# Optimization experiments

Measured on AMD Instinct MI355X. Metric: run time of the kernel, lower is better.

The kernel has to match this reference:

```python
import jax, jax.numpy as jnp
import numpy as np

B, C, H, W = 4, 256, 64, 64
INTER = max(1, C // 8)  # 32


def setup_inputs() -> dict:
    key = jax.random.key(0)
    ks = jax.random.split(key, 8)
    s = 0.02  # conv weight init scale
    return {
        "feat": jax.random.normal(ks[0], (B, C, H, W), jnp.float32),
        "edge": jax.random.normal(ks[1], (B, C, H, W), jnp.float32),
        "wq": jax.random.normal(ks[2], (INTER, C), jnp.float32) * s,
        "bq": jnp.zeros((INTER,), jnp.float32),
        "wk": jax.random.normal(ks[3], (INTER, C), jnp.float32) * s,
        "bk": jnp.zeros((INTER,), jnp.float32),
        "wv": jax.random.normal(ks[4], (C, C), jnp.float32) * s,
        "bv": jnp.zeros((C,), jnp.float32),
    }


def reference(feat, edge, wq, bq, wk, bk, wv, bv):
    b, c, h, w = feat.shape
    n = h * w
    # 1x1 convs as channel matmuls; flatten spatial dims to n = H*W tokens
    q = (jnp.einsum('ic,bchw->bihw', wq, feat) + bq[None, :, None, None]).reshape(b, -1, n)  # [B, inter, N]
    k = (jnp.einsum('ic,bchw->bihw', wk, edge) + bk[None, :, None, None]).reshape(b, -1, n)  # [B, inter, N]
    v = (jnp.einsum('oc,bchw->bohw', wv, edge) + bv[None, :, None, None]).reshape(b, c, n)   # [B, C, N]
    # scores[b, nq, nk] = sum_i q[b,i,nq] * k[b,i,nk]; softmax over nk
    attn = jax.nn.softmax(jnp.einsum('bin,bim->bnm', q, k), axis=-1)  # [B, N, N]
    # out[b,c,nq] = sum_m v[b,c,m] * attn[b,nq,m]
    out = jnp.einsum('bcm,bnm->bcn', v, attn).reshape(b, c, h, w)
    return out + feat
```

## Files before the change

### kernel.cpp

```cpp
#include <hip/hip_runtime.h>
#include <cstddef>

#define BB 4
#define CC 256
#define NN 4096
#define NI 32

typedef __attribute__((ext_vector_type(8))) short bf16x8;
typedef __attribute__((ext_vector_type(16))) float f32x16;
typedef __attribute__((ext_vector_type(4))) float f32x4;
typedef unsigned short ushort_t;
typedef unsigned int uint32;

typedef union { uint32 u[4]; bf16x8 v; } fragU;

__device__ __forceinline__ uint32 f2bf_bits(float f) {
    union { float f; uint32 u; } v; v.f = f;
    return (v.u + 0x7fffu + ((v.u >> 16) & 1u)) >> 16;
}
__device__ __forceinline__ uint32 pack2bf(float a, float b) {
    return f2bf_bits(a) | (f2bf_bits(b) << 16);
}
__device__ __forceinline__ uint32 pack2bf_t(float a, float b) {
    union { float f; uint32 u; } A, B; A.f = a; B.f = b;
    return (B.u & 0xFFFF0000u) | (A.u >> 16);
}

__device__ __forceinline__ size_t vfidx(int b, int n, int c) {
    return ((((size_t)b * (NN / 16) + (n >> 4)) * 2 + ((n >> 3) & 1)) * (CC * 8))
           + (size_t)c * 8 + (n & 7);
}

__global__ __launch_bounds__(256) void wconv_kernel(
    const float* __restrict__ wq, const float* __restrict__ wk,
    const float* __restrict__ wv,
    ushort_t* __restrict__ wqF, ushort_t* __restrict__ wkF,
    ushort_t* __restrict__ wvF)
{
    const int bid = blockIdx.x;
    const int t = threadIdx.x;
    if (bid < 64) {
        const int fi = bid * 256 + t;
        const int o  = fi >> 6;
        const int k4 = (fi & 63) * 4;
        const f32x4 x = *(const f32x4*)&wv[(size_t)o * CC + k4];
        const int kkg = k4 >> 4, hh = (k4 >> 3) & 1, j0 = k4 & 7;
        const int ot = o >> 5, lane = hh * 32 + (o & 31);
        uint2 p; p.x = pack2bf(x[0], x[1]); p.y = pack2bf(x[2], x[3]);
        *(uint2*)&wvF[((size_t)(ot * 16 + kkg) * 64 + lane) * 8 + j0] = p;
    } else {
        const int which = (bid - 64) >> 1;
        const int part  = (bid - 64) & 1;
        const float* src = which ? wk : wq;
        ushort_t* dst = which ? wkF : wqF;
#pragma unroll
        for (int p = 0; p < 4; ++p) {
            const int fi = part * 1024 + p * 256 + t;
            const int o  = fi >> 6;
            const int k4 = (fi & 63) * 4;
            const f32x4 x = *(const f32x4*)&src[(size_t)o * CC + k4];
            const int kkg = k4 >> 4, hh = (k4 >> 3) & 1, j0 = k4 & 7;
            const int lane = hh * 32 + (o & 31);
            uint2 pr; pr.x = pack2bf(x[0], x[1]); pr.y = pack2bf(x[2], x[3]);
            *(uint2*)&dst[((size_t)kkg * 64 + lane) * 8 + j0] = pr;
        }
    }
}

__global__ __launch_bounds__(256, 1) void proj_kernel(
    const float* __restrict__ feat, const float* __restrict__ edge,
    const ushort_t* __restrict__ wqF, const ushort_t* __restrict__ wkF,
    const ushort_t* __restrict__ wvF,
    const float* __restrict__ bq, const float* __restrict__ bk,
    const float* __restrict__ bv,
    ushort_t* __restrict__ qT, ushort_t* __restrict__ kT,
    ushort_t* __restrict__ vF)
{
    __shared__ __attribute__((aligned(16))) uint32 sF[4][2][64][4];
    __shared__ __attribute__((aligned(16))) uint32 sE[4][2][64][4];

    const int tid = threadIdx.x;
    const int b = blockIdx.y;
    const int n0 = blockIdx.x * 64;
    const int w = tid >> 6, lane = tid & 63;
    const int col = lane & 31, h = lane >> 5;

    const ushort_t* __restrict__ aQK = ((w < 2) ? wqF : wkF) + (size_t)lane * 8;
    const ushort_t* __restrict__ wvB0 = wvF + ((size_t)((2 * w + 0) * 16) * 64 + lane) * 8;
    const ushort_t* __restrict__ wvB1 = wvF + ((size_t)((2 * w + 1) * 16) * 64 + lane) * 8;
    const uint32* __restrict__ bSrc =
        (w == 0) ? &sF[0][0][lane][0] :
        (w == 1) ? &sF[0][1][lane][0] :
        (w == 2) ? &sE[0][0][lane][0] : &sE[0][1][lane][0];

    f32x16 accV[2][2];
    f32x16 accS;
#pragma unroll
    for (int r = 0; r < 16; ++r) {
        accS[r] = 0.f;
        accV[0][0][r] = 0.f; accV[0][1][r] = 0.f;
        accV[1][0][r] = 0.f; accV[1][1][r] = 0.f;
    }

    f32x4 rF[2][2], rE[2][2];

#pragma unroll
    for (int p = 0; p < 2; ++p) {
        const int pi = p * 256 + tid;
        const int m = pi >> 4, cidx = pi & 15;
        const size_t ga = ((size_t)(b * CC + 2 * m)) * NN + n0 + cidx * 4;
        rF[p][0] = *(const f32x4*)&feat[ga];
        rF[p][1] = *(const f32x4*)&feat[ga + NN];
        rE[p][0] = *(const f32x4*)&edge[ga];
        rE[p][1] = *(const f32x4*)&edge[ga + NN];
    }

    for (int ch = 0; ch < 4; ++ch) {
#pragma unroll
        for (int p = 0; p < 2; ++p) {
            const int pi = p * 256 + tid;
            const int m = pi >> 4, cidx = pi & 15;
            const int kk = m >> 3, hh = (m >> 2) & 1, ju = m & 3;
#pragma unroll
            for (int c = 0; c < 4; ++c) {
                const int cn = cidx * 4 + c;
                const int nt = cn >> 5, cl = cn & 31;
                sF[kk][nt][hh * 32 + cl][ju] = pack2bf(rF[p][0][c], rF[p][1][c]);
                sE[kk][nt][hh * 32 + cl][ju] = pack2bf(rE[p][0][c], rE[p][1][c]);
            }
        }
        __syncthreads();

        if (ch < 3) {
            const int c0 = (ch + 1) * 64;
#pragma unroll
            for (int p = 0; p < 2; ++p) {
                const int pi = p * 256 + tid;
                const int m = pi >> 4, cidx = pi & 15;
                const size_t ga = ((size_t)(b * CC + c0 + 2 * m)) * NN + n0 + cidx * 4;
                rF[p][0] = *(const f32x4*)&feat[ga];
                rF[p][1] = *(const f32x4*)&feat[ga + NN];
                rE[p][0] = *(const f32x4*)&edge[ga];
                rE[p][1] = *(const f32x4*)&edge[ga + NN];
            }
        }

#pragma unroll
        for (int kk = 0; kk < 4; ++kk) {
            const int kkg = ch * 4 + kk;
            const bf16x8 eA0 = *(const bf16x8*)&sE[kk][0][lane][0];
            const bf16x8 eA1 = *(const bf16x8*)&sE[kk][1][lane][0];
            const bf16x8 vB0 = *(const bf16x8*)&wvB0[(size_t)kkg * 512];
            const bf16x8 vB1 = *(const bf16x8*)&wvB1[(size_t)kkg * 512];
            const bf16x8 aS  = *(const bf16x8*)&aQK[(size_t)kkg * 512];
            const bf16x8 bS  = *(const bf16x8*)&bSrc[(size_t)kk * 512];
            accS = __builtin_amdgcn_mfma_f32_32x32x16_bf16(aS, bS, accS, 0, 0, 0);
            accV[0][0] = __builtin_amdgcn_mfma_f32_32x32x16_bf16(eA0, vB0, accV[0][0], 0, 0, 0);
            accV[0][1] = __builtin_amdgcn_mfma_f32_32x32x16_bf16(eA0, vB1, accV[0][1], 0, 0, 0);
            accV[1][0] = __builtin_amdgcn_mfma_f32_32x32x16_bf16(eA1, vB0, accV[1][0], 0, 0, 0);
            accV[1][1] = __builtin_amdgcn_mfma_f32_32x32x16_bf16(eA1, vB1, accV[1][1], 0, 0, 0);
        }
        __syncthreads();
    }

    {
        const float* bias = (w < 2) ? bq : bk;
        ushort_t* dst = (w < 2) ? qT : kT;
        const int nt = w & 1;
        const size_t base = ((size_t)b * NN + n0 + nt * 32 + col) * NI;
#pragma unroll
        for (int q = 0; q < 4; ++q) {
            const int i0 = 8 * q + 4 * h;
            const float x0 = accS[4 * q + 0] + bias[i0 + 0];
            const float x1 = accS[4 * q + 1] + bias[i0 + 1];
            const float x2 = accS[4 * q + 2] + bias[i0 + 2];
            const float x3 = accS[4 * q + 3] + bias[i0 + 3];
            uint2 pr; pr.x = pack2bf(x0, x1); pr.y = pack2bf(x2, x3);
            *(uint2*)&dst[base + i0] = pr;
        }
    }

#pragma unroll
    for (int cti = 0; cti < 2; ++cti) {
        const int o = (2 * w + cti) * 32 + col;
        const float vb = bv[o];
#pragma unroll
        for (int mt = 0; mt < 2; ++mt) {
#pragma unroll
            for (int q = 0; q < 4; ++q) {
                const int nst = n0 + mt * 32 + 8 * q + 4 * h;
                uint2 pr;
                pr.x = pack2bf(accV[mt][cti][4 * q + 0] + vb,
                               accV[mt][cti][4 * q + 1] + vb);
                pr.y = pack2bf(accV[mt][cti][4 * q + 2] + vb,
                               accV[mt][cti][4 * q + 3] + vb);
                *(uint2*)&vF[vfidx(b, nst, o)] = pr;
            }
        }
    }
}

__global__ __launch_bounds__(512, 2) void attn_kernel(
    const ushort_t* __restrict__ qT, const ushort_t* __restrict__ kT,
    const ushort_t* __restrict__ vF, const float* __restrict__ feat,
    float* __restrict__ out)
{
    __shared__ float red[4][64][33];
    __shared__ float lpart[4][2][32];
    __shared__ float linvS[64];

    const int tid  = threadIdx.x;
    const int b    = blockIdx.y;
    const int nq0  = blockIdx.x * 64;
    const int w    = tid >> 6;
    const int lane = tid & 63;
    const int col  = lane & 31;
    const int h    = lane >> 5;
    const int qs   = w & 1;
    const int kg   = w >> 1;

    bf16x8 bQ0, bQ1;
    {
        const size_t qb = ((size_t)b * NN + nq0 + qs * 32 + col) * NI + h * 8;
        bQ0 = *(const bf16x8*)&qT[qb];
        bQ1 = *(const bf16x8*)&qT[qb + 16];
    }

    f32x16 acc[8];
#pragma unroll
    for (int cs = 0; cs < 8; ++cs)
#pragma unroll
        for (int r = 0; r < 16; ++r) acc[cs][r] = 0.f;

    float lp = 0.f;

    const size_t kTb = (size_t)b * NN * NI;
    const int keybase = kg * 1024;

    for (int strip = 0; strip < 32; ++strip) {
        const int key0 = keybase + strip * 32;

        const size_t kb = kTb + (size_t)(key0 + col) * NI + h * 8;
        const bf16x8 aK0 = *(const bf16x8*)&kT[kb];
        const bf16x8 aK1 = *(const bf16x8*)&kT[kb + 16];

        f32x16 st;
#pragma unroll
        for (int r = 0; r < 16; ++r) st[r] = 0.f;
        st = __builtin_amdgcn_mfma_f32_32x32x16_bf16(aK0, bQ0, st, 0, 0, 0);
        st = __builtin_amdgcn_mfma_f32_32x32x16_bf16(aK1, bQ1, st, 0, 0, 0);

        float p[16]; float sum = 0.f;
#pragma unroll
        for (int r = 0; r < 16; ++r) { p[r] = __expf(st[r]); sum += p[r]; }
        lp += sum;

        uint32 pk[8];
#pragma unroll
        for (int j = 0; j < 8; ++j) pk[j] = pack2bf_t(p[2 * j], p[2 * j + 1]);
        uint32 rv[8];
#pragma unroll
        for (int j = 0; j < 8; ++j) rv[j] = __shfl_xor(pk[j], 32, 64);
        fragU F0, F1;
        F0.u[0] = h ? rv[2] : pk[0];
        F0.u[1] = h ? rv[3] : pk[1];
        F0.u[2] = h ? pk[2] : rv[0];
        F0.u[3] = h ? pk[3] : rv[1];
        F1.u[0] = h ? rv[6] : pk[4];
        F1.u[1] = h ? rv[7] : pk[5];
        F1.u[2] = h ? pk[6] : rv[4];
        F1.u[3] = h ? pk[7] : rv[5];

        const size_t vbB = (((size_t)b * (NN / 16) + (key0 >> 4)) * 2 + h) * (CC * 8)
                         + (size_t)col * 8;
#pragma unroll
        for (int cs = 0; cs < 8; ++cs) {
            const bf16x8 v0 = *(const bf16x8*)&vF[vbB + cs * 256];
            const bf16x8 v1 = *(const bf16x8*)&vF[vbB + 4096 + cs * 256];
            acc[cs] = __builtin_amdgcn_mfma_f32_32x32x16_bf16(F0.v, v0, acc[cs], 0, 0, 0);
            acc[cs] = __builtin_amdgcn_mfma_f32_32x32x16_bf16(F1.v, v1, acc[cs], 0, 0, 0);
        }
    }

    lp += __shfl_xor(lp, 32, 64);
    if (h == 0) lpart[kg][qs][col] = lp;
    __syncthreads();
    if (tid < 64) {
        const int s = tid >> 5, q = tid & 31;
        linvS[tid] = 1.0f / (lpart[0][s][q] + lpart[1][s][q] + lpart[2][s][q] + lpart[3][s][q]);
    }
    __syncthreads();

    const int c32 = tid >> 4;
    const int q4  = (tid & 15) * 4;
    float lv[4];
#pragma unroll
    for (int j = 0; j < 4; ++j) lv[j] = linvS[q4 + j];

#pragma unroll
    for (int pp = 0; pp < 8; ++pp) {
#pragma unroll
        for (int r = 0; r < 16; ++r) {
            const int row = qs * 32 + (r & 3) + 8 * (r >> 2) + 4 * h;
            red[kg][row][col] = acc[pp][r];
        }
        __syncthreads();
        {
            const int cglob = pp * 32 + c32;
            const size_t gb = ((size_t)b * CC + cglob) * NN + nq0 + q4;
            float o[4];
#pragma unroll
            for (int j = 0; j < 4; ++j)
                o[j] = red[0][q4 + j][c32] + red[1][q4 + j][c32]
                     + red[2][q4 + j][c32] + red[3][q4 + j][c32];
            const float4 f4 = *(const float4*)&feat[gb];
            float4 o4;
            o4.x = o[0] * lv[0] + f4.x;
            o4.y = o[1] * lv[1] + f4.y;
            o4.z = o[2] * lv[2] + f4.z;
            o4.w = o[3] * lv[3] + f4.w;
            *(float4*)&out[gb] = o4;
        }
        __syncthreads();
    }
}

extern "C" void kernel_launch(void* const* d_in, const int* in_sizes, int n_in,
                              void* d_out, int out_size, void* d_ws, size_t ws_size,
                              hipStream_t stream)
{
    (void)in_sizes; (void)n_in; (void)out_size; (void)ws_size;
    const float* feat = (const float*)d_in[0];
    const float* edge = (const float*)d_in[1];
    const float* wq   = (const float*)d_in[2];
    const float* bq   = (const float*)d_in[3];
    const float* wk   = (const float*)d_in[4];
    const float* bk   = (const float*)d_in[5];
    const float* wv   = (const float*)d_in[6];
    const float* bv   = (const float*)d_in[7];
    float* out = (float*)d_out;

    ushort_t* qT  = (ushort_t*)d_ws;
    ushort_t* kT  = qT + (size_t)BB * NN * NI;
    ushort_t* vF  = kT + (size_t)BB * NN * NI;

    ushort_t* wvF = (ushort_t*)d_out;
    ushort_t* wqF = wvF + (size_t)CC * CC;
    ushort_t* wkF = wqF + (size_t)NI * CC;

    wconv_kernel<<<dim3(68), 256, 0, stream>>>(wq, wk, wv, wqF, wkF, wvF);
    proj_kernel<<<dim3(NN / 64, BB), 256, 0, stream>>>(feat, edge, wqF, wkF, wvF,
                                                       bq, bk, bv, qT, kT, vF);
    attn_kernel<<<dim3(NN / 64, BB), 512, 0, stream>>>(qT, kT, vF, feat, out);
}
```

Before: 152.4 us.

## Fold log2e into Q weights, prefetch K, set MFMA priority, remap attention grid

Folds log2(e) into the Q projection weights and bias so the softmax can use the native exp2 instead of __expf. The next K strip is now loaded during the current strip's work to hide its load latency. s_setprio is raised around the PV MFMA loop. The attention grid is flattened to 1D with a block-index swizzle that interleaves batches, meant to change which blocks share K/V in L2. Rounding q to bf16 after scaling changes numerics slightly, and the prefetch adds register pressure to a kernel already holding 128 accumulator floats.

```diff
diff --git a/kernel.cpp b/kernel.cpp
--- a/kernel.cpp
+++ b/kernel.cpp
@@ -5,6 +5,7 @@
 #define CC 256
 #define NN 4096
 #define NI 32
+#define LOG2E 1.4426950408889634f
 
 typedef __attribute__((ext_vector_type(8))) short bf16x8;
 typedef __attribute__((ext_vector_type(16))) float f32x16;
@@ -53,6 +54,7 @@
         const int part  = (bid - 64) & 1;
         const float* src = which ? wk : wq;
         ushort_t* dst = which ? wkF : wqF;
+        const float sc = which ? 1.0f : LOG2E;
 #pragma unroll
         for (int p = 0; p < 4; ++p) {
             const int fi = part * 1024 + p * 256 + t;
@@ -61,7 +63,8 @@
             const f32x4 x = *(const f32x4*)&src[(size_t)o * CC + k4];
             const int kkg = k4 >> 4, hh = (k4 >> 3) & 1, j0 = k4 & 7;
             const int lane = hh * 32 + (o & 31);
-            uint2 pr; pr.x = pack2bf(x[0], x[1]); pr.y = pack2bf(x[2], x[3]);
+            uint2 pr; pr.x = pack2bf(x[0] * sc, x[1] * sc);
+            pr.y = pack2bf(x[2] * sc, x[3] * sc);
             *(uint2*)&dst[((size_t)kkg * 64 + lane) * 8 + j0] = pr;
         }
     }
@@ -165,16 +168,17 @@
 
     {
         const float* bias = (w < 2) ? bq : bk;
+        const float bsc = (w < 2) ? LOG2E : 1.0f;
         ushort_t* dst = (w < 2) ? qT : kT;
         const int nt = w & 1;
         const size_t base = ((size_t)b * NN + n0 + nt * 32 + col) * NI;
 #pragma unroll
         for (int q = 0; q < 4; ++q) {
             const int i0 = 8 * q + 4 * h;
-            const float x0 = accS[4 * q + 0] + bias[i0 + 0];
-            const float x1 = accS[4 * q + 1] + bias[i0 + 1];
-            const float x2 = accS[4 * q + 2] + bias[i0 + 2];
-            const float x3 = accS[4 * q + 3] + bias[i0 + 3];
+            const float x0 = accS[4 * q + 0] + bias[i0 + 0] * bsc;
+            const float x1 = accS[4 * q + 1] + bias[i0 + 1] * bsc;
+            const float x2 = accS[4 * q + 2] + bias[i0 + 2] * bsc;
+            const float x3 = accS[4 * q + 3] + bias[i0 + 3] * bsc;
             uint2 pr; pr.x = pack2bf(x0, x1); pr.y = pack2bf(x2, x3);
             *(uint2*)&dst[base + i0] = pr;
         }
@@ -210,8 +214,9 @@
     __shared__ float linvS[64];
 
     const int tid  = threadIdx.x;
-    const int b    = blockIdx.y;
-    const int nq0  = blockIdx.x * 64;
+    const int id   = blockIdx.x;
+    const int b    = (id & 7) >> 1;
+    const int nq0  = (((id >> 3) << 1) | (id & 1)) * 64;
     const int w    = tid >> 6;
     const int lane = tid & 63;
     const int col  = lane & 31;
@@ -237,12 +242,15 @@
     const size_t kTb = (size_t)b * NN * NI;
     const int keybase = kg * 1024;
 
+    bf16x8 aK0, aK1;
+    {
+        const size_t kb = kTb + (size_t)(keybase + col) * NI + h * 8;
+        aK0 = *(const bf16x8*)&kT[kb];
+        aK1 = *(const bf16x8*)&kT[kb + 16];
+    }
+
     for (int strip = 0; strip < 32; ++strip) {
         const int key0 = keybase + strip * 32;
-
-        const size_t kb = kTb + (size_t)(key0 + col) * NI + h * 8;
-        const bf16x8 aK0 = *(const bf16x8*)&kT[kb];
-        const bf16x8 aK1 = *(const bf16x8*)&kT[kb + 16];
 
         f32x16 st;
 #pragma unroll
@@ -250,9 +258,19 @@
         st = __builtin_amdgcn_mfma_f32_32x32x16_bf16(aK0, bQ0, st, 0, 0, 0);
         st = __builtin_amdgcn_mfma_f32_32x32x16_bf16(aK1, bQ1, st, 0, 0, 0);
 
+        bf16x8 nK0, nK1;
+        if (strip < 31) {
+            const size_t kbn = kTb + (size_t)(key0 + 32 + col) * NI + h * 8;
+            nK0 = *(const bf16x8*)&kT[kbn];
+            nK1 = *(const bf16x8*)&kT[kbn + 16];
+        }
+
         float p[16]; float sum = 0.f;
 #pragma unroll
-        for (int r = 0; r < 16; ++r) { p[r] = __expf(st[r]); sum += p[r]; }
+        for (int r = 0; r < 16; ++r) {
+            p[r] = __builtin_amdgcn_exp2f(st[r]);
+            sum += p[r];
+        }
         lp += sum;
 
         uint32 pk[8];
@@ -273,6 +291,7 @@
 
         const size_t vbB = (((size_t)b * (NN / 16) + (key0 >> 4)) * 2 + h) * (CC * 8)
                          + (size_t)col * 8;
+        __builtin_amdgcn_s_setprio(1);
 #pragma unroll
         for (int cs = 0; cs < 8; ++cs) {
             const bf16x8 v0 = *(const bf16x8*)&vF[vbB + cs * 256];
@@ -280,6 +299,9 @@
             acc[cs] = __builtin_amdgcn_mfma_f32_32x32x16_bf16(F0.v, v0, acc[cs], 0, 0, 0);
             acc[cs] = __builtin_amdgcn_mfma_f32_32x32x16_bf16(F1.v, v1, acc[cs], 0, 0, 0);
         }
+        __builtin_amdgcn_s_setprio(0);
+
+        if (strip < 31) { aK0 = nK0; aK1 = nK1; }
     }
 
     lp += __shfl_xor(lp, 32, 64);
@@ -287,7 +309,8 @@
     __syncthreads();
     if (tid < 64) {
         const int s = tid >> 5, q = tid & 31;
-        linvS[tid] = 1.0f / (lpart[0][s][q] + lpart[1][s][q] + lpart[2][s][q] + lpart[3][s][q]);
+        linvS[tid] = 1.0f / (lpart[0][s][q] + lpart[1][s][q]
+                           + lpart[2][s][q] + lpart[3][s][q]);
     }
     __syncthreads();
 
@@ -351,5 +374,5 @@
     wconv_kernel<<<dim3(68), 256, 0, stream>>>(wq, wk, wv, wqF, wkF, wvF);
     proj_kernel<<<dim3(NN / 64, BB), 256, 0, stream>>>(feat, edge, wqF, wkF, wvF,
                                                        bq, bk, bv, qT, kT, vF);
-    attn_kernel<<<dim3(NN / 64, BB), 512, 0, stream>>>(qT, kT, vF, feat, out);
-}
+    attn_kernel<<<dim3(NN / 64 * BB), 512, 0, stream>>>(qT, kT, vF, feat, out);
+}
```

New measurement: 193.3 us. 26.8% more time.
